# Optimization experiments

Measured on AMD Instinct MI355X. Metric: run time of the kernel, lower is better.

## Reference

```python
import jax, jax.numpy as jnp
import numpy as np

N_NODES = 10000
N_EDGES = 100000
IN_FEATS = 64
OUT_FEATS = 64
N_EDGE_TYPES = 10


def setup_inputs() -> dict:
    key = jax.random.key(0)
    k_feat, k_src, k_dst, k_ord, k_emb = jax.random.split(key, 5)
    feat = jax.random.normal(k_feat, (N_NODES, IN_FEATS), dtype=jnp.float32)
    src = jax.random.randint(k_src, (N_EDGES,), 0, N_NODES, dtype=jnp.int32)
    dst = jax.random.randint(k_dst, (N_EDGES,), 0, N_NODES, dtype=jnp.int32)
    order = jax.random.randint(k_ord, (N_EDGES,), 0, N_EDGE_TYPES, dtype=jnp.int32)
    # xavier-uniform-like init for the relation-weight embedding table
    emb_weight = jax.random.normal(k_emb, (N_EDGE_TYPES, IN_FEATS * OUT_FEATS), dtype=jnp.float32) * 0.02
    bias = jnp.zeros((OUT_FEATS,), dtype=jnp.float32)
    return {"feat": feat, "src": src, "dst": dst, "order": order,
            "emb_weight": emb_weight, "bias": bias}


def reference(feat, src, dst, order, emb_weight, bias):
    n_nodes, in_feats = feat.shape
    out_feats = emb_weight.shape[1] // in_feats
    n_edges = src.shape[0]
    ones_e = jnp.ones((n_edges,), dtype=feat.dtype)

    # norm='both': scale source features by out_degree^{-1/2}
    out_deg = jnp.clip(jax.ops.segment_sum(ones_e, src, num_segments=n_nodes), 1.0)
    feat_n = feat * (out_deg ** -0.5)[:, None]

    # per-edge relation weight gather: [E, out, in]
    w = emb_weight[order].reshape(n_edges, out_feats, in_feats)
    h_src = feat_n[src]                              # [E, in]
    msg = jnp.einsum('eoi,ei->eo', w, h_src)         # [E, out]

    # scatter-sum aggregate to destination nodes
    rst = jax.ops.segment_sum(msg, dst, num_segments=n_nodes)  # [N, out]

    # post-norm by in_degree^{-1/2}
    in_deg = jnp.clip(jax.ops.segment_sum(ones_e, dst, num_segments=n_nodes), 1.0)
    rst = rst * (in_deg ** -0.5)[:, None]
    return rst + bias
```

## Files before the change

kernel.cpp:

```cpp
#include <hip/hip_runtime.h>
#include <stdint.h>


typedef __attribute__((ext_vector_type(8))) short short8;
typedef __attribute__((ext_vector_type(4))) float f32x4;

constexpr int N_NODES = 10000;
constexpr int N_EDGES = 100000;
constexpr int F = 64;
constexpr int R = 10;
constexpr int BLOCK = 256;
constexpr int EPG = 32;
constexpr int CAP = 16384;
constexpr int CAPN = 64;
constexpr int MAXG = N_EDGES / EPG + R;

union U8 { uint32_t u[4]; short8 s; };

__device__ inline uint32_t pk_hi(float x, float y) {
    uint32_t bx = __float_as_uint(x), by = __float_as_uint(y);
    return (bx >> 16) | (by & 0xFFFF0000u);
}
__device__ inline uint32_t pk_lo(float x, float y) {
    uint32_t bx = __float_as_uint(x), by = __float_as_uint(y);
    float lx = x - __uint_as_float(bx & 0xFFFF0000u);
    float ly = y - __uint_as_float(by & 0xFFFF0000u);
    return (__float_as_uint(lx) >> 16) | (__float_as_uint(ly) & 0xFFFF0000u);
}

__global__ void k_count(const int* __restrict__ src, const int* __restrict__ dst,
                        const int* __restrict__ order, const float* __restrict__ emb,
                        const float* __restrict__ feat,
                        unsigned* deg_out, unsigned* deg_in, unsigned* rel_cnt,
                        int* __restrict__ ssrc, uint4* __restrict__ wfrag,
                        int* __restrict__ dstbuf, uint4* __restrict__ pfeat) {
    __shared__ int hist[R], base[R];
    unsigned sent = rel_cnt[15];
    int tid = threadIdx.x;
    int t = blockIdx.x * BLOCK + tid;
    if (tid < R) hist[tid] = 0;
    __syncthreads();
    int r = -1, lr = 0, s = 0, d = 0, rank = 0;
    if (t < N_EDGES) {
        s = src[t]; d = dst[t];
        atomicAdd(&deg_out[s], 1u);
        rank = (int)(atomicAdd(&deg_in[d], 1u) - sent);
        r = order[t];
        lr = atomicAdd(&hist[r], 1);
    }
    __syncthreads();
    if (tid < R)
        base[tid] = hist[tid] ? (int)(atomicAdd(&rel_cnt[tid], (unsigned)hist[tid]) - sent) : 0;
    __syncthreads();
    if (t < N_EDGES) {
        int slot = r * CAP + base[r] + lr;
        ssrc[slot] = s;
        if (rank < CAPN) dstbuf[d * CAPN + rank] = slot;
    }

    if (t < R * 16 * 64) {
        int lane = t & 63, frag = t >> 6;
        int p = frag & 1, ks = (frag >> 1) & 1, tt = (frag >> 2) & 3, rr = frag >> 4;
        int o = 16 * tt + (lane & 15), q = lane >> 4;
        const float* w = emb + (size_t)rr * F * F + (size_t)o * F + 32 * ks + 8 * q;
        float4 f0 = *(const float4*)w;
        float4 f1 = *(const float4*)(w + 4);
        uint4 v;
        if (p == 0) v = make_uint4(pk_hi(f0.x, f0.y), pk_hi(f0.z, f0.w),
                                   pk_hi(f1.x, f1.y), pk_hi(f1.z, f1.w));
        else        v = make_uint4(pk_lo(f0.x, f0.y), pk_lo(f0.z, f0.w),
                                   pk_lo(f1.x, f1.y), pk_lo(f1.z, f1.w));
        wfrag[(size_t)frag * 64 + lane] = v;
    }

    if (t < N_NODES * 4) {
        int n = t >> 2, p = t & 3;
        const float* rp = feat + (size_t)n * F + 16 * p;
        float4 a = *(const float4*)rp;
        float4 b = *(const float4*)(rp + 4);
        float4 c = *(const float4*)(rp + 8);
        float4 e = *(const float4*)(rp + 12);
        uint4* pf = pfeat + (size_t)n * 16;
        pf[2 * p]     = make_uint4(pk_hi(a.x, a.y), pk_hi(a.z, a.w),
                                   pk_hi(b.x, b.y), pk_hi(b.z, b.w));
        pf[2 * p + 1] = make_uint4(pk_hi(c.x, c.y), pk_hi(c.z, c.w),
                                   pk_hi(e.x, e.y), pk_hi(e.z, e.w));
        pf[8 + 2 * p]     = make_uint4(pk_lo(a.x, a.y), pk_lo(a.z, a.w),
                                       pk_lo(b.x, b.y), pk_lo(b.z, b.w));
        pf[8 + 2 * p + 1] = make_uint4(pk_lo(c.x, c.y), pk_lo(c.z, c.w),
                                       pk_lo(e.x, e.y), pk_lo(e.z, e.w));
    }
}

__global__ __launch_bounds__(BLOCK, 3) void k_edge(
    const uint4* __restrict__ pfeat, const unsigned* __restrict__ deg_out,
    const short8* __restrict__ wfrag, const unsigned* __restrict__ rel_cnt,
    const int* __restrict__ ssrc, float* __restrict__ msg) {
    int lane = threadIdx.x & 63;
    int wib = threadIdx.x >> 6;
    int g = blockIdx.x * (BLOCK / 64) + wib;
    unsigned sent = rel_cnt[15];

    int r = -1, lg = 0, cnt = 0, cum = 0;
#pragma unroll
    for (int i = 0; i < R; ++i) {
        int ci = (int)(rel_cnt[i] - sent);
        int gi = (ci + EPG - 1) >> 5;
        if (g >= cum && g < cum + gi) { r = i; lg = g - cum; cnt = ci; }
        cum += gi;
    }
    if (r < 0) return;
    int e0 = lg << 5;

    int q = lane >> 4;
    int iA = e0 + (lane & 15), iB = iA + 16;
    const int* sr = ssrc + r * CAP;
    int sA = iA < cnt ? sr[iA] : 0;
    int sB = iB < cnt ? sr[iB] : 0;

    float nrA = rsqrtf((float)max((int)(deg_out[sA] - sent), 1));
    float nrB = rsqrtf((float)max((int)(deg_out[sB] - sent), 1));

    const short8* pA = (const short8*)(pfeat + (size_t)sA * 16);
    const short8* pB = (const short8*)(pfeat + (size_t)sB * 16);
    short8 Ah0 = pA[q], Ah1 = pA[4 + q], Al0 = pA[8 + q], Al1 = pA[12 + q];
    short8 Bh0 = pB[q], Bh1 = pB[4 + q], Bl0 = pB[8 + q], Bl1 = pB[12 + q];

    const short8* wf = wfrag + (size_t)r * 16 * 64;
    f32x4 acc0[4], acc1[4];
#pragma unroll
    for (int t = 0; t < 4; ++t) {
        acc0[t] = (f32x4){0.f, 0.f, 0.f, 0.f};
        acc1[t] = (f32x4){0.f, 0.f, 0.f, 0.f};
    }

#pragma unroll
    for (int t = 0; t < 4; ++t) {
        short8 bh0 = wf[(t * 4 + 0) * 64 + lane];
        short8 bl0 = wf[(t * 4 + 1) * 64 + lane];
        short8 bh1 = wf[(t * 4 + 2) * 64 + lane];
        short8 bl1 = wf[(t * 4 + 3) * 64 + lane];
        f32x4 x = acc0[t], y = acc1[t];
        x = __builtin_amdgcn_mfma_f32_16x16x32_bf16(Al0, bh0, x, 0, 0, 0);
        y = __builtin_amdgcn_mfma_f32_16x16x32_bf16(Bl0, bh0, y, 0, 0, 0);
        x = __builtin_amdgcn_mfma_f32_16x16x32_bf16(Ah0, bl0, x, 0, 0, 0);
        y = __builtin_amdgcn_mfma_f32_16x16x32_bf16(Bh0, bl0, y, 0, 0, 0);
        x = __builtin_amdgcn_mfma_f32_16x16x32_bf16(Ah0, bh0, x, 0, 0, 0);
        y = __builtin_amdgcn_mfma_f32_16x16x32_bf16(Bh0, bh0, y, 0, 0, 0);
        x = __builtin_amdgcn_mfma_f32_16x16x32_bf16(Al1, bh1, x, 0, 0, 0);
        y = __builtin_amdgcn_mfma_f32_16x16x32_bf16(Bl1, bh1, y, 0, 0, 0);
        x = __builtin_amdgcn_mfma_f32_16x16x32_bf16(Ah1, bl1, x, 0, 0, 0);
        y = __builtin_amdgcn_mfma_f32_16x16x32_bf16(Bh1, bl1, y, 0, 0, 0);
        x = __builtin_amdgcn_mfma_f32_16x16x32_bf16(Ah1, bh1, x, 0, 0, 0);
        y = __builtin_amdgcn_mfma_f32_16x16x32_bf16(Bh1, bh1, y, 0, 0, 0);
        acc0[t] = x; acc1[t] = y;
    }

    float* mrow = msg + ((size_t)(r * CAP + e0)) * F;
    int col = lane & 15;
#pragma unroll
    for (int gg = 0; gg < 4; ++gg) {
        int row = q * 4 + gg;
        float rA = __shfl(nrA, row);
        float rB = __shfl(nrB, row);
#pragma unroll
        for (int t = 0; t < 4; ++t) {
            mrow[row * F + 16 * t + col] = acc0[t][gg] * rA;
            mrow[(row + 16) * F + 16 * t + col] = acc1[t][gg] * rB;
        }
    }
}

__global__ void k_agg(const float4* __restrict__ msg, const int* __restrict__ dstbuf,
                      const unsigned* __restrict__ deg_in,
                      const unsigned* __restrict__ rel_cnt,
                      const float* __restrict__ bias, float4* __restrict__ out) {
    int t = blockIdx.x * BLOCK + threadIdx.x;
    if (t >= N_NODES * 16) return;
    unsigned sent = rel_cnt[15];
    int n = t >> 4, c4 = t & 15;
    int deg = (int)(deg_in[n] - sent);
    const int* dl = dstbuf + (size_t)n * CAPN;
    float4 acc = make_float4(0.f, 0.f, 0.f, 0.f);
    int k = 0;
    for (; k + 4 <= deg; k += 4) {
        int s0 = dl[k], s1 = dl[k + 1], s2 = dl[k + 2], s3 = dl[k + 3];
        float4 g0 = msg[(size_t)s0 * 16 + c4];
        float4 g1 = msg[(size_t)s1 * 16 + c4];
        float4 g2 = msg[(size_t)s2 * 16 + c4];
        float4 g3 = msg[(size_t)s3 * 16 + c4];
        acc.x += (g0.x + g1.x) + (g2.x + g3.x);
        acc.y += (g0.y + g1.y) + (g2.y + g3.y);
        acc.z += (g0.z + g1.z) + (g2.z + g3.z);
        acc.w += (g0.w + g1.w) + (g2.w + g3.w);
    }
    for (; k < deg; ++k) {
        float4 g = msg[(size_t)dl[k] * 16 + c4];
        acc.x += g.x; acc.y += g.y; acc.z += g.z; acc.w += g.w;
    }
    float sc = rsqrtf((float)max(deg, 1));
    float4 b = ((const float4*)bias)[c4];
    out[t] = make_float4(acc.x * sc + b.x, acc.y * sc + b.y,
                         acc.z * sc + b.z, acc.w * sc + b.w);
}

extern "C" void kernel_launch(void* const* d_in, const int* in_sizes, int n_in,
                              void* d_out, int out_size, void* d_ws, size_t ws_size,
                              hipStream_t stream) {
    const float* feat  = (const float*)d_in[0];
    const int*   src   = (const int*)d_in[1];
    const int*   dst   = (const int*)d_in[2];
    const int*   order = (const int*)d_in[3];
    const float* emb   = (const float*)d_in[4];
    const float* bias  = (const float*)d_in[5];
    float* out = (float*)d_out;

    unsigned* deg_out = (unsigned*)d_ws;
    unsigned* deg_in  = deg_out + N_NODES;
    unsigned* rel_cnt = deg_in + N_NODES;
    int*   ssrc    = (int*)(rel_cnt + 16);
    uint4* wfrag   = (uint4*)(ssrc + R * CAP);
    int*   dstbuf  = (int*)(wfrag + (size_t)R * 16 * 64);
    uint4* pfeat   = (uint4*)(dstbuf + (size_t)N_NODES * CAPN);
    float* msg     = (float*)(pfeat + (size_t)N_NODES * 16);

    int eb = (N_EDGES + BLOCK - 1) / BLOCK;
    k_count<<<eb, BLOCK, 0, stream>>>(src, dst, order, emb, feat, deg_out, deg_in,
                                      rel_cnt, ssrc, wfrag, dstbuf, pfeat);
    int gblocks = (MAXG + (BLOCK / 64) - 1) / (BLOCK / 64);
    k_edge<<<gblocks, BLOCK, 0, stream>>>(pfeat, deg_out, (const short8*)wfrag,
                                          rel_cnt, ssrc, msg);
    int ab = (N_NODES * 16 + BLOCK - 1) / BLOCK;
    k_agg<<<ab, BLOCK, 0, stream>>>((const float4*)msg, dstbuf, deg_in, rel_cnt,
                                    bias, (float4*)out);
}
```

Baseline: 103.1 us.

## Precompute per-relation node transforms instead of per-edge bucketed GEMMs

Replaces the per-edge relation-bucketed GEMM with a dense per-(relation,node) transform: every node's normalized features are multiplied by all 10 relation weights, and the aggregator gathers the row for (relation, src) per incoming edge. This removes the shared-memory histogram, the relation bucket counting and the source scatter from the count kernel, and gives the GEMM a regular 2D grid. In exchange it does 10x10000 node transforms instead of 100000 edge transforms, roughly the same work, and keeps a similarly sized message buffer. It also clamps the aggregation loop to the in-edge list capacity.

```diff
diff --git a/kernel.cpp b/kernel.cpp
--- a/kernel.cpp
+++ b/kernel.cpp
@@ -10,10 +10,9 @@
 constexpr int F = 64;
 constexpr int R = 10;
 constexpr int BLOCK = 256;
-constexpr int EPG = 32;
-constexpr int CAP = 16384;
 constexpr int CAPN = 64;
-constexpr int MAXG = N_EDGES / EPG + R;
+constexpr int WPR = (N_NODES + 31) / 32;
+constexpr int GBX = (WPR + (BLOCK / 64) - 1) / (BLOCK / 64);
 
 union U8 { uint32_t u[4]; short8 s; };
 
@@ -31,31 +30,19 @@
 __global__ void k_count(const int* __restrict__ src, const int* __restrict__ dst,
                         const int* __restrict__ order, const float* __restrict__ emb,
                         const float* __restrict__ feat,
-                        unsigned* deg_out, unsigned* deg_in, unsigned* rel_cnt,
-                        int* __restrict__ ssrc, uint4* __restrict__ wfrag,
-                        int* __restrict__ dstbuf, uint4* __restrict__ pfeat) {
-    __shared__ int hist[R], base[R];
-    unsigned sent = rel_cnt[15];
-    int tid = threadIdx.x;
-    int t = blockIdx.x * BLOCK + tid;
-    if (tid < R) hist[tid] = 0;
-    __syncthreads();
-    int r = -1, lr = 0, s = 0, d = 0, rank = 0;
+                        unsigned* deg_out, unsigned* deg_in,
+                        const unsigned* __restrict__ sent_ptr,
+                        uint4* __restrict__ wfrag, int* __restrict__ dstbuf,
+                        uint4* __restrict__ pfeat) {
+    unsigned sent = *sent_ptr;
+    int t = blockIdx.x * BLOCK + threadIdx.x;
+
     if (t < N_EDGES) {
-        s = src[t]; d = dst[t];
+        int s = src[t], d = dst[t], r = order[t];
         atomicAdd(&deg_out[s], 1u);
-        rank = (int)(atomicAdd(&deg_in[d], 1u) - sent);
-        r = order[t];
-        lr = atomicAdd(&hist[r], 1);
-    }
-    __syncthreads();
-    if (tid < R)
-        base[tid] = hist[tid] ? (int)(atomicAdd(&rel_cnt[tid], (unsigned)hist[tid]) - sent) : 0;
-    __syncthreads();
-    if (t < N_EDGES) {
-        int slot = r * CAP + base[r] + lr;
-        ssrc[slot] = s;
-        if (rank < CAPN) dstbuf[d * CAPN + rank] = slot;
+        int rank = (int)(atomicAdd(&deg_in[d], 1u) - sent);
+        if (rank < CAPN)
+            dstbuf[d * CAPN + rank] = r * N_NODES + s;
     }
 
     if (t < R * 16 * 64) {
@@ -92,37 +79,26 @@
     }
 }
 
-__global__ __launch_bounds__(BLOCK, 3) void k_edge(
+__global__ __launch_bounds__(BLOCK, 3) void k_gemm(
     const uint4* __restrict__ pfeat, const unsigned* __restrict__ deg_out,
-    const short8* __restrict__ wfrag, const unsigned* __restrict__ rel_cnt,
-    const int* __restrict__ ssrc, float* __restrict__ msg) {
+    const unsigned* __restrict__ sent_ptr, const short8* __restrict__ wfrag,
+    float* __restrict__ msg) {
     int lane = threadIdx.x & 63;
     int wib = threadIdx.x >> 6;
-    int g = blockIdx.x * (BLOCK / 64) + wib;
-    unsigned sent = rel_cnt[15];
-
-    int r = -1, lg = 0, cnt = 0, cum = 0;
-#pragma unroll
-    for (int i = 0; i < R; ++i) {
-        int ci = (int)(rel_cnt[i] - sent);
-        int gi = (ci + EPG - 1) >> 5;
-        if (g >= cum && g < cum + gi) { r = i; lg = g - cum; cnt = ci; }
-        cum += gi;
-    }
-    if (r < 0) return;
-    int e0 = lg << 5;
+    int r = blockIdx.y;
+    int base = (blockIdx.x * (BLOCK / 64) + wib) * 32;
+    if (base >= N_NODES) return;
+    unsigned sent = *sent_ptr;
 
     int q = lane >> 4;
-    int iA = e0 + (lane & 15), iB = iA + 16;
-    const int* sr = ssrc + r * CAP;
-    int sA = iA < cnt ? sr[iA] : 0;
-    int sB = iB < cnt ? sr[iB] : 0;
-
-    float nrA = rsqrtf((float)max((int)(deg_out[sA] - sent), 1));
-    float nrB = rsqrtf((float)max((int)(deg_out[sB] - sent), 1));
-
-    const short8* pA = (const short8*)(pfeat + (size_t)sA * 16);
-    const short8* pB = (const short8*)(pfeat + (size_t)sB * 16);
+    int nA = base + (lane & 15), nB = nA + 16;
+    int cA = min(nA, N_NODES - 1), cB = min(nB, N_NODES - 1);
+
+    float nrA = rsqrtf((float)max((int)(deg_out[cA] - sent), 1));
+    float nrB = rsqrtf((float)max((int)(deg_out[cB] - sent), 1));
+
+    const short8* pA = (const short8*)(pfeat + (size_t)cA * 16);
+    const short8* pB = (const short8*)(pfeat + (size_t)cB * 16);
     short8 Ah0 = pA[q], Ah1 = pA[4 + q], Al0 = pA[8 + q], Al1 = pA[12 + q];
     short8 Bh0 = pB[q], Bh1 = pB[4 + q], Bl0 = pB[8 + q], Bl1 = pB[12 + q];
 
@@ -156,34 +132,37 @@
         acc0[t] = x; acc1[t] = y;
     }
 
-    float* mrow = msg + ((size_t)(r * CAP + e0)) * F;
+    float* mrow = msg + ((size_t)r * N_NODES + base) * F;
     int col = lane & 15;
 #pragma unroll
     for (int gg = 0; gg < 4; ++gg) {
         int row = q * 4 + gg;
         float rA = __shfl(nrA, row);
         float rB = __shfl(nrB, row);
+        bool okA = base + row < N_NODES;
+        bool okB = base + 16 + row < N_NODES;
 #pragma unroll
         for (int t = 0; t < 4; ++t) {
-            mrow[row * F + 16 * t + col] = acc0[t][gg] * rA;
-            mrow[(row + 16) * F + 16 * t + col] = acc1[t][gg] * rB;
+            if (okA) mrow[row * F + 16 * t + col] = acc0[t][gg] * rA;
+            if (okB) mrow[(row + 16) * F + 16 * t + col] = acc1[t][gg] * rB;
         }
     }
 }
 
 __global__ void k_agg(const float4* __restrict__ msg, const int* __restrict__ dstbuf,
                       const unsigned* __restrict__ deg_in,
-                      const unsigned* __restrict__ rel_cnt,
+                      const unsigned* __restrict__ sent_ptr,
                       const float* __restrict__ bias, float4* __restrict__ out) {
     int t = blockIdx.x * BLOCK + threadIdx.x;
     if (t >= N_NODES * 16) return;
-    unsigned sent = rel_cnt[15];
+    unsigned sent = *sent_ptr;
     int n = t >> 4, c4 = t & 15;
     int deg = (int)(deg_in[n] - sent);
+    int lim = min(deg, CAPN);
     const int* dl = dstbuf + (size_t)n * CAPN;
     float4 acc = make_float4(0.f, 0.f, 0.f, 0.f);
     int k = 0;
-    for (; k + 4 <= deg; k += 4) {
+    for (; k + 4 <= lim; k += 4) {
         int s0 = dl[k], s1 = dl[k + 1], s2 = dl[k + 2], s3 = dl[k + 3];
         float4 g0 = msg[(size_t)s0 * 16 + c4];
         float4 g1 = msg[(size_t)s1 * 16 + c4];
@@ -194,7 +173,7 @@
         acc.z += (g0.z + g1.z) + (g2.z + g3.z);
         acc.w += (g0.w + g1.w) + (g2.w + g3.w);
     }
-    for (; k < deg; ++k) {
+    for (; k < lim; ++k) {
         float4 g = msg[(size_t)dl[k] * 16 + c4];
         acc.x += g.x; acc.y += g.y; acc.z += g.z; acc.w += g.w;
     }
@@ -217,20 +196,19 @@
 
     unsigned* deg_out = (unsigned*)d_ws;
     unsigned* deg_in  = deg_out + N_NODES;
-    unsigned* rel_cnt = deg_in + N_NODES;
-    int*   ssrc    = (int*)(rel_cnt + 16);
-    uint4* wfrag   = (uint4*)(ssrc + R * CAP);
+    unsigned* sent    = deg_in + N_NODES;
+    uint4* wfrag   = (uint4*)(sent + 16);
     int*   dstbuf  = (int*)(wfrag + (size_t)R * 16 * 64);
     uint4* pfeat   = (uint4*)(dstbuf + (size_t)N_NODES * CAPN);
     float* msg     = (float*)(pfeat + (size_t)N_NODES * 16);
 
     int eb = (N_EDGES + BLOCK - 1) / BLOCK;
     k_count<<<eb, BLOCK, 0, stream>>>(src, dst, order, emb, feat, deg_out, deg_in,
-                                      rel_cnt, ssrc, wfrag, dstbuf, pfeat);
-    int gblocks = (MAXG + (BLOCK / 64) - 1) / (BLOCK / 64);
-    k_edge<<<gblocks, BLOCK, 0, stream>>>(pfeat, deg_out, (const short8*)wfrag,
-                                          rel_cnt, ssrc, msg);
+                                      sent, wfrag, dstbuf, pfeat);
+    dim3 gg(GBX, R);
+    k_gemm<<<gg, BLOCK, 0, stream>>>(pfeat, deg_out, sent, (const short8*)wfrag,
+                                     msg);
     int ab = (N_NODES * 16 + BLOCK - 1) / BLOCK;
-    k_agg<<<ab, BLOCK, 0, stream>>>((const float4*)msg, dstbuf, deg_in, rel_cnt,
+    k_agg<<<ab, BLOCK, 0, stream>>>((const float4*)msg, dstbuf, deg_in, sent,
                                     bias, (float4*)out);
 }
```

Result: faster. 100.5 us (-2.5%).
